# Kernel optimization log

Hardware: AMD Instinct MI355X
Metric: run time of the kernel (lower is better)

## Reference

```python
import jax, jax.numpy as jnp
import numpy as np

B, C, H, W = 8, 64, 64, 64
OUT_H, OUT_W = 32, 32


def setup_inputs() -> dict:
    key = jax.random.key(0)
    ks = jax.random.split(key, 9)
    s = 1.0 / np.sqrt(C).astype(np.float32)
    return {
        "x": jax.random.normal(ks[0], (B, C, H, W), jnp.float32),
        "wq": jax.random.normal(ks[1], (C, C), jnp.float32) * s,
        "bq": jax.random.normal(ks[2], (C,), jnp.float32) * 0.01,
        "wk": jax.random.normal(ks[3], (C, C), jnp.float32) * s,
        "bk": jax.random.normal(ks[4], (C,), jnp.float32) * 0.01,
        "wv": jax.random.normal(ks[5], (C, C), jnp.float32) * s,
        "bv": jax.random.normal(ks[6], (C,), jnp.float32) * 0.01,
        "wm": jax.random.normal(ks[7], (C, C), jnp.float32) * s,
        "bm": jax.random.normal(ks[8], (C,), jnp.float32) * 0.01,
    }


def reference(x, wq, bq, wk, bk, wv, bv, wm, bm):
    # pushforward: self-attention over spatial tokens, 1x1-conv mixing + ReLU,
    # then bilinear resize to out_shape (align_corners=False semantics).
    b, c, h, w = x.shape
    t = x.reshape(b, c, h * w).transpose(0, 2, 1)  # [B, HW, C] tokens
    q = jnp.einsum('bnc,dc->bnd', t, wq) + bq      # 1x1 conv == per-pixel linear
    k = jnp.einsum('bnc,dc->bnd', t, wk) + bk
    v = jnp.einsum('bnc,dc->bnd', t, wv) + bv
    scores = jnp.einsum('bnc,bmc->bnm', q, k) / jnp.sqrt(jnp.float32(c))  # [B, HW, HW]
    attn = jax.nn.softmax(scores, axis=-1)
    o = jnp.einsum('bnm,bmc->bnc', attn, v)        # [B, HW, C]
    mixed = jax.nn.relu(jnp.einsum('bnc,dc->bnd', o, wm) + bm)
    out = mixed.transpose(0, 2, 1).reshape(b, c, h, w)
    # F.interpolate(mode='bilinear', align_corners=False) == half-pixel bilinear, no antialias
    out = jax.image.resize(out, (b, c, OUT_H, OUT_W), method='bilinear', antialias=False)
    return out
```

## Files before the change

kernel.cpp:

```cpp
#include <hip/hip_runtime.h>
#include <stdint.h>

typedef unsigned short u16;
typedef unsigned int   u32;
typedef __attribute__((ext_vector_type(8)))  short short8;
typedef __attribute__((ext_vector_type(4)))  float f32x4;
typedef __attribute__((ext_vector_type(16))) float f32x16;

#define NTOK 4096
#define LOG2E 1.44269504088896340736f
#define QS    (0.125f * LOG2E)

__device__ __forceinline__ u16 f2bf(float f) {
    u32 u = __builtin_bit_cast(u32, f);
    u += 0x7fffu + ((u >> 16) & 1u);
    return (u16)(u >> 16);
}
__device__ __forceinline__ float bf2f(u16 v) {
    return __builtin_bit_cast(float, (u32)v << 16);
}
__device__ __forceinline__ u32 pk_hu(float a, float b) {
    u32 ua = __builtin_bit_cast(u32, a) + 0x8000u;
    u32 ub = __builtin_bit_cast(u32, b) + 0x8000u;
    return __builtin_amdgcn_perm(ub, ua, 0x07060302);
}
__device__ __forceinline__ f32x16 zero16() {
    f32x16 v;
#pragma unroll
    for (int i = 0; i < 16; ++i) v[i] = 0.f;
    return v;
}

#define MFMA16x32 __builtin_amdgcn_mfma_f32_16x16x32_bf16
#define MFMA32x16 __builtin_amdgcn_mfma_f32_32x32x16_bf16

__global__ __launch_bounds__(256) void qkv_mfma4(
    const float* __restrict__ x,
    const float* __restrict__ wq, const float* __restrict__ bq,
    const float* __restrict__ wk, const float* __restrict__ bk,
    const float* __restrict__ wv, const float* __restrict__ bv,
    u16* __restrict__ Q, u16* __restrict__ K, u16* __restrict__ Vp)
{
    __shared__ __align__(16) u16 Wl[3 * 64 * 72];
    __shared__ __align__(16) u16 Xl[64 * 64];
    const int tid  = threadIdx.x;
    const int b    = blockIdx.x & 7;
    const int slab = blockIdx.x >> 3;
    const int n0   = slab << 6;
    const int wave = tid >> 6;
    const int lane = tid & 63;
    const int quad = lane >> 4;
    const int l15  = lane & 15;

#pragma unroll
    for (int j = 0; j < 12; ++j) {
        const float* src = (j < 4) ? wq : (j < 8) ? wk : wv;
        const float sc = (j < 4) ? QS : 1.0f;
        const int idx = (j & 3) * 1024 + tid * 4;
        const float4 v = *(const float4*)(src + idx);
        uint2 pk;
        pk.x = (u32)f2bf(v.x * sc) | ((u32)f2bf(v.y * sc) << 16);
        pk.y = (u32)f2bf(v.z * sc) | ((u32)f2bf(v.w * sc) << 16);
        *(uint2*)&Wl[(j >> 2) * 4608 + (idx >> 6) * 72 + (idx & 63)] = pk;
    }

    float4 xs[4];
#pragma unroll
    for (int g = 0; g < 4; ++g) {
        const int ch = g * 16 + wave * 4 + quad;
        xs[g] = *(const float4*)(x + ((size_t)(b * 64 + ch)) * NTOK + n0 + l15 * 4);
    }
#pragma unroll
    for (int g = 0; g < 4; ++g) {
        const int ch = g * 16 + wave * 4 + quad;
        const float vv[4] = {xs[g].x, xs[g].y, xs[g].z, xs[g].w};
#pragma unroll
        for (int e = 0; e < 4; ++e) {
            const int tok = l15 * 4 + e;
            Xl[tok * 64 + (((ch >> 3) ^ (tok & 7)) & 7) * 8 + (ch & 7)] = f2bf(vv[e]);
        }
    }
    __syncthreads();

    const int row0 = wave * 16 + l15;
    short8 xf[2];
#pragma unroll
    for (int kk = 0; kk < 2; ++kk)
        xf[kk] = *(const short8*)&Xl[row0 * 64 + (((kk * 4 + quad) ^ (row0 & 7)) & 7) * 8];

    const size_t tokbase = (size_t)b * NTOK + n0 + wave * 16;

#pragma unroll
    for (int mat = 0; mat < 2; ++mat) {
        const float* bias = (mat == 0) ? bq : bk;
        const float bsc = (mat == 0) ? QS : 1.0f;
#pragma unroll
        for (int mt = 0; mt < 4; ++mt) {
            const u16* wr = &Wl[mat * 4608 + (mt * 16 + l15) * 72 + quad * 8];
            const short8 wf0 = *(const short8*)(wr);
            const short8 wf1 = *(const short8*)(wr + 32);
            f32x4 acc = {0.f, 0.f, 0.f, 0.f};
            acc = MFMA16x32(wf0, xf[0], acc, 0, 0, 0);
            acc = MFMA16x32(wf1, xf[1], acc, 0, 0, 0);
            const float4 b4 = *(const float4*)(bias + mt * 16 + quad * 4);
            uint2 pk;
            pk.x = (u32)f2bf(acc[0] + b4.x * bsc) | ((u32)f2bf(acc[1] + b4.y * bsc) << 16);
            pk.y = (u32)f2bf(acc[2] + b4.z * bsc) | ((u32)f2bf(acc[3] + b4.w * bsc) << 16);
            u16* dst = (mat == 0) ? Q : K;
            *(uint2*)(dst + (tokbase + l15) * 64 + mt * 16 + quad * 4) = pk;
        }
    }

    __syncthreads();
    u16* Vl = Xl;
    const int tok = wave * 16 + l15;
#pragma unroll
    for (int mt = 0; mt < 4; ++mt) {
        const u16* wr = &Wl[2 * 4608 + (mt * 16 + l15) * 72 + quad * 8];
        const short8 wf0 = *(const short8*)(wr);
        const short8 wf1 = *(const short8*)(wr + 32);
        f32x4 acc = {0.f, 0.f, 0.f, 0.f};
        acc = MFMA16x32(wf0, xf[0], acc, 0, 0, 0);
        acc = MFMA16x32(wf1, xf[1], acc, 0, 0, 0);
        const float4 b4 = *(const float4*)(bv + mt * 16 + quad * 4);
        const float o[4] = {acc[0] + b4.x, acc[1] + b4.y, acc[2] + b4.z, acc[3] + b4.w};
#pragma unroll
        for (int r = 0; r < 4; ++r) {
            const int d = mt * 16 + quad * 4 + r;
            Vl[d * 64 + (((tok >> 3) ^ ((d >> 1) & 7)) & 7) * 8 + (tok & 7)] = f2bf(o[r]);
        }
    }
    __syncthreads();

#pragma unroll
    for (int dd = 0; dd < 4; ++dd) {
        const int d2   = (tid >> 4) + dd * 16;
        const int tok0 = (tid & 15) * 4;
        const int slot = ((tok0 >> 3) ^ ((d2 >> 1) & 7)) & 7;
        const uint2 v2 = *(const uint2*)&Vl[d2 * 64 + slot * 8 + (tok0 & 7)];
        const int gt = slab * 2 + (tok0 >> 5);
        *(uint2*)(Vp + (((size_t)b * 128 + gt) * 64 + d2) * 32 + (tok0 & 31)) = v2;
    }
}

__global__ __launch_bounds__(512, 2) void attn7(
    const u16* __restrict__ Q, const u16* __restrict__ K,
    const u16* __restrict__ Vp,
    const float* __restrict__ wm, const float* __restrict__ bm,
    float* __restrict__ out)
{
    __shared__ __align__(16) char smem[54272];
    const int tid  = threadIdx.x;
    const int wave = tid >> 6;
    const int lane = tid & 63;
    const int c31  = lane & 31;
    const int hw   = lane >> 5;
    const int quad = lane >> 4;
    const int l15  = lane & 15;
    const int h    = wave >> 2;
    const int s    = wave & 3;
    const int b    = blockIdx.x & 7;
    const int oh   = blockIdx.x >> 3;
    const int n0   = oh * 128;

    short8 qf[2][4];
#pragma unroll
    for (int nt = 0; nt < 2; ++nt)
#pragma unroll
        for (int ks = 0; ks < 4; ++ks)
            qf[nt][ks] = *(const short8*)(Q + ((size_t)(b * NTOK + n0 + h * 64 + nt * 32 + c31)) * 64
                                            + ks * 16 + hw * 8);

    const u16* Kb  = K + ((size_t)b * NTOK + s * 1024) * 64;
    const u16* Vbp = Vp + ((size_t)b * 128 + s * 32) * 2048;

    f32x16 O[2][2];
#pragma unroll
    for (int mt = 0; mt < 2; ++mt)
#pragma unroll
        for (int nt = 0; nt < 2; ++nt) O[mt][nt] = zero16();
    float lpa[2] = {0.f, 0.f};

    auto load_kv = [&](short8 (&kf)[4], short8 (&vf)[4], int t) {
        const int tc = (t < 32) ? t : 31;
        const u16* kt = Kb + (size_t)tc * 2048;
#pragma unroll
        for (int ks = 0; ks < 4; ++ks)
            kf[ks] = *(const short8*)(kt + c31 * 64 + ks * 16 + hw * 8);
        const u16* vt = Vbp + (size_t)tc * 2048;
#pragma unroll
        for (int mk = 0; mk < 4; ++mk)
            vf[mk] = *(const short8*)(vt + ((mk >> 1) * 32 + c31) * 32 + (mk & 1) * 16 + hw * 8);
    };

    auto tile_tail = [&](const f32x16 (&sv)[2], const short8 (&vf)[4]) {
#pragma unroll
        for (int nt = 0; nt < 2; ++nt) {
            float p[16];
#pragma unroll
            for (int r = 0; r < 16; ++r) p[r] = __builtin_amdgcn_exp2f(sv[nt][r]);
            lpa[nt] += (((p[0] + p[1]) + (p[2] + p[3])) + ((p[4] + p[5]) + (p[6] + p[7])))
                     + (((p[8] + p[9]) + (p[10] + p[11])) + ((p[12] + p[13]) + (p[14] + p[15])));
            u32 g[8];
#pragma unroll
            for (int gi = 0; gi < 8; ++gi) g[gi] = pk_hu(p[2 * gi], p[2 * gi + 1]);
            const u32 rA = __shfl_xor(hw ? g[0] : g[2], 32);
            const u32 rB = __shfl_xor(hw ? g[1] : g[3], 32);
            const u32 rC = __shfl_xor(hw ? g[4] : g[6], 32);
            const u32 rD = __shfl_xor(hw ? g[5] : g[7], 32);
            uint4 B0, B1;
            B0.x = hw ? rA : g[0];  B0.y = hw ? rB : g[1];
            B0.z = hw ? g[2] : rA;  B0.w = hw ? g[3] : rB;
            B1.x = hw ? rC : g[4];  B1.y = hw ? rD : g[5];
            B1.z = hw ? g[6] : rC;  B1.w = hw ? g[7] : rD;
            const short8 pb0 = __builtin_bit_cast(short8, B0);
            const short8 pb1 = __builtin_bit_cast(short8, B1);
            O[0][nt] = MFMA32x16(vf[0], pb0, O[0][nt], 0, 0, 0);
            O[0][nt] = MFMA32x16(vf[1], pb1, O[0][nt], 0, 0, 0);
            O[1][nt] = MFMA32x16(vf[2], pb0, O[1][nt], 0, 0, 0);
            O[1][nt] = MFMA32x16(vf[3], pb1, O[1][nt], 0, 0, 0);
        }
    };

    short8 kfA[4], vfA[4], kfB[4], vfB[4];
    load_kv(kfA, vfA, 0);

#pragma unroll 1
    for (int tt = 0; tt < 16; ++tt) {
        const int t0 = tt * 2;
        f32x16 sv0[2];
#pragma unroll
        for (int nt = 0; nt < 2; ++nt) {
            f32x16 a = zero16();
            a = MFMA32x16(kfA[0], qf[nt][0], a, 0, 0, 0);
            a = MFMA32x16(kfA[1], qf[nt][1], a, 0, 0, 0);
            a = MFMA32x16(kfA[2], qf[nt][2], a, 0, 0, 0);
            a = MFMA32x16(kfA[3], qf[nt][3], a, 0, 0, 0);
            sv0[nt] = a;
        }
        load_kv(kfB, vfB, t0 + 1);
        tile_tail(sv0, vfA);

        f32x16 sv1[2];
#pragma unroll
        for (int nt = 0; nt < 2; ++nt) {
            f32x16 a = zero16();
            a = MFMA32x16(kfB[0], qf[nt][0], a, 0, 0, 0);
            a = MFMA32x16(kfB[1], qf[nt][1], a, 0, 0, 0);
            a = MFMA32x16(kfB[2], qf[nt][2], a, 0, 0, 0);
            a = MFMA32x16(kfB[3], qf[nt][3], a, 0, 0, 0);
            sv1[nt] = a;
        }
        load_kv(kfA, vfA, t0 + 2);
        tile_tail(sv1, vfB);
    }

#pragma unroll
    for (int nt = 0; nt < 2; ++nt) lpa[nt] += __shfl_xor(lpa[nt], 32);

    float* lpbuf = (float*)(smem + 52224);
    if (hw == 0) {
#pragma unroll
        for (int nt = 0; nt < 2; ++nt)
            lpbuf[(h * 4 + s) * 64 + nt * 32 + c31] = lpa[nt];
    }
    if (s != 0) {
        u16* sec = (u16*)smem + (h * 3 + s - 1) * 4352;
#pragma unroll
        for (int mt = 0; mt < 2; ++mt)
#pragma unroll
            for (int nt = 0; nt < 2; ++nt)
#pragma unroll
                for (int r = 0; r < 16; ++r) {
                    const int ch = mt * 32 + (r & 3) + 8 * (r >> 2) + 4 * hw;
                    sec[(nt * 32 + c31) * 68 + ch] = f2bf(O[mt][nt][r]);
                }
    }
    __syncthreads();

    float rinv[2];
    if (s == 0) {
#pragma unroll
        for (int nt = 0; nt < 2; ++nt) {
            float sum = 0.f;
#pragma unroll
            for (int sx = 0; sx < 4; ++sx)
                sum += lpbuf[(h * 4 + sx) * 64 + nt * 32 + c31];
            rinv[nt] = 1.0f / sum;
        }
#pragma unroll
        for (int sx = 1; sx < 4; ++sx) {
            const u16* sec = (const u16*)smem + (h * 3 + sx - 1) * 4352;
#pragma unroll
            for (int mt = 0; mt < 2; ++mt)
#pragma unroll
                for (int nt = 0; nt < 2; ++nt)
#pragma unroll
                    for (int r = 0; r < 16; ++r) {
                        const int ch = mt * 32 + (r & 3) + 8 * (r >> 2) + 4 * hw;
                        O[mt][nt][r] += bf2f(sec[(nt * 32 + c31) * 68 + ch]);
                    }
        }
    }
    short8 wB[4][2];
    float bb[4];
#pragma unroll
    for (int nt = 0; nt < 4; ++nt) {
        const int d = nt * 16 + l15;
        const float* wr = wm + (size_t)d * 64 + quad * 8;
        const float4 a0 = *(const float4*)(wr);
        const float4 a1 = *(const float4*)(wr + 4);
        const float4 c0 = *(const float4*)(wr + 32);
        const float4 c1 = *(const float4*)(wr + 36);
        ((u32*)&wB[nt][0])[0] = pk_hu(a0.y, a0.x) ^ 0u, ((u32*)&wB[nt][0])[0] = (u32)f2bf(a0.x) | ((u32)f2bf(a0.y) << 16);
        ((u32*)&wB[nt][0])[1] = (u32)f2bf(a0.z) | ((u32)f2bf(a0.w) << 16);
        ((u32*)&wB[nt][0])[2] = (u32)f2bf(a1.x) | ((u32)f2bf(a1.y) << 16);
        ((u32*)&wB[nt][0])[3] = (u32)f2bf(a1.z) | ((u32)f2bf(a1.w) << 16);
        ((u32*)&wB[nt][1])[0] = (u32)f2bf(c0.x) | ((u32)f2bf(c0.y) << 16);
        ((u32*)&wB[nt][1])[1] = (u32)f2bf(c0.z) | ((u32)f2bf(c0.w) << 16);
        ((u32*)&wB[nt][1])[2] = (u32)f2bf(c1.x) | ((u32)f2bf(c1.y) << 16);
        ((u32*)&wB[nt][1])[3] = (u32)f2bf(c1.z) | ((u32)f2bf(c1.w) << 16);
        bb[nt] = bm[d];
    }
    __syncthreads();

    if (s == 0) {
        u16* M0 = (u16*)smem + h * 4096;
#pragma unroll
        for (int mt = 0; mt < 2; ++mt)
#pragma unroll
            for (int nt = 0; nt < 2; ++nt)
#pragma unroll
                for (int r = 0; r < 16; ++r) {
                    const int lr = nt * 32 + c31;
                    const int ch = mt * 32 + (r & 3) + 8 * (r >> 2) + 4 * hw;
                    const float v = O[mt][nt][r] * rinv[nt];
                    M0[lr * 64 + (((ch >> 3) ^ (lr & 7)) & 7) * 8 + (ch & 7)] = f2bf(v);
                }
    }
    __syncthreads();

    const u16* M0r = (const u16*)smem + (wave >> 2) * 4096;
    const int lr = (wave & 3) * 16 + l15;
    const short8 af0 = *(const short8*)&M0r[lr * 64 + ((quad ^ (lr & 7)) & 7) * 8];
    const short8 af1 = *(const short8*)&M0r[lr * 64 + (((4 + quad) ^ (lr & 7)) & 7) * 8];
    float* Mf = (float*)(smem + 16384);
#pragma unroll
    for (int nt = 0; nt < 4; ++nt) {
        f32x4 acc = {0.f, 0.f, 0.f, 0.f};
        acc = MFMA16x32(af0, wB[nt][0], acc, 0, 0, 0);
        acc = MFMA16x32(af1, wB[nt][1], acc, 0, 0, 0);
#pragma unroll
        for (int r = 0; r < 4; ++r) {
            float v = acc[r] + bb[nt];
            v = v > 0.f ? v : 0.f;
            Mf[(wave * 16 + quad * 4 + r) * 68 + nt * 16 + l15] = v;
        }
    }
    __syncthreads();

    const int ow = tid & 31;
    const int cb = (tid >> 5) & 15;
#pragma unroll
    for (int i = 0; i < 4; ++i) {
        const int c = cb + i * 16;
        const float v = 0.25f * (Mf[(2 * ow) * 68 + c] + Mf[(2 * ow + 1) * 68 + c]
                               + Mf[(64 + 2 * ow) * 68 + c] + Mf[(65 + 2 * ow) * 68 + c]);
        out[((size_t)(b * 64 + c) * 32 + oh) * 32 + ow] = v;
    }
}

extern "C" void kernel_launch(void* const* d_in, const int* in_sizes, int n_in,
                              void* d_out, int out_size, void* d_ws, size_t ws_size,
                              hipStream_t stream) {
    (void)in_sizes; (void)n_in; (void)out_size; (void)ws_size;
    const float* x  = (const float*)d_in[0];
    const float* wq = (const float*)d_in[1];
    const float* bq = (const float*)d_in[2];
    const float* wk = (const float*)d_in[3];
    const float* bk = (const float*)d_in[4];
    const float* wv = (const float*)d_in[5];
    const float* bv = (const float*)d_in[6];
    const float* wm = (const float*)d_in[7];
    const float* bm = (const float*)d_in[8];

    u16* Q  = (u16*)d_ws;
    u16* K  = Q + (size_t)8 * NTOK * 64;
    u16* Vp = K + (size_t)8 * NTOK * 64;

    qkv_mfma4<<<512, 256, 0, stream>>>(x, wq, bq, wk, bk, wv, bv, Q, K, Vp);
    attn7<<<256, 512, 0, stream>>>(Q, K, Vp, wm, bm, (float*)d_out);
}
```

Baseline: 137.2 us.

## Split KV sequence across eight waves per query group with 1024-thread blocks

Doubles the block to 1024 threads so each query group's key/value sequence is split eight ways instead of four, halving per-wave loop length and doubling waves in flight. The split-K reduction, softmax normalization and output-mixing stages are reworked for the larger block, and LDS stores/loads become packed 64-bit. Per-block LDS rises to about 123KB, so occupancy is limited to one block per CU, and the serial reduction over seven partial sums by wave 0 grows.

```diff
diff --git a/kernel.cpp b/kernel.cpp
--- a/kernel.cpp
+++ b/kernel.cpp
@@ -143,13 +143,13 @@
     }
 }
 
-__global__ __launch_bounds__(512, 2) void attn7(
+__global__ __launch_bounds__(1024, 4) void attn8(
     const u16* __restrict__ Q, const u16* __restrict__ K,
     const u16* __restrict__ Vp,
     const float* __restrict__ wm, const float* __restrict__ bm,
     float* __restrict__ out)
 {
-    __shared__ __align__(16) char smem[54272];
+    __shared__ __align__(16) char smem[125952];
     const int tid  = threadIdx.x;
     const int wave = tid >> 6;
     const int lane = tid & 63;
@@ -157,8 +157,8 @@
     const int hw   = lane >> 5;
     const int quad = lane >> 4;
     const int l15  = lane & 15;
-    const int h    = wave >> 2;
-    const int s    = wave & 3;
+    const int h    = wave >> 3;
+    const int s    = wave & 7;
     const int b    = blockIdx.x & 7;
     const int oh   = blockIdx.x >> 3;
     const int n0   = oh * 128;
@@ -171,8 +171,8 @@
             qf[nt][ks] = *(const short8*)(Q + ((size_t)(b * NTOK + n0 + h * 64 + nt * 32 + c31)) * 64
                                             + ks * 16 + hw * 8);
 
-    const u16* Kb  = K + ((size_t)b * NTOK + s * 1024) * 64;
-    const u16* Vbp = Vp + ((size_t)b * 128 + s * 32) * 2048;
+    const u16* Kb  = K + ((size_t)b * NTOK + s * 512) * 64;
+    const u16* Vbp = Vp + ((size_t)b * 128 + s * 16) * 2048;
 
     f32x16 O[2][2];
 #pragma unroll
@@ -182,7 +182,7 @@
     float lpa[2] = {0.f, 0.f};
 
     auto load_kv = [&](short8 (&kf)[4], short8 (&vf)[4], int t) {
-        const int tc = (t < 32) ? t : 31;
+        const int tc = (t < 16) ? t : 15;
         const u16* kt = Kb + (size_t)tc * 2048;
 #pragma unroll
         for (int ks = 0; ks < 4; ++ks)
@@ -226,7 +226,7 @@
     load_kv(kfA, vfA, 0);
 
 #pragma unroll 1
-    for (int tt = 0; tt < 16; ++tt) {
+    for (int tt = 0; tt < 8; ++tt) {
         const int t0 = tt * 2;
         f32x16 sv0[2];
 #pragma unroll
@@ -258,22 +258,26 @@
 #pragma unroll
     for (int nt = 0; nt < 2; ++nt) lpa[nt] += __shfl_xor(lpa[nt], 32);
 
-    float* lpbuf = (float*)(smem + 52224);
+    float* lpbuf = (float*)(smem + 121856);
     if (hw == 0) {
 #pragma unroll
         for (int nt = 0; nt < 2; ++nt)
-            lpbuf[(h * 4 + s) * 64 + nt * 32 + c31] = lpa[nt];
+            lpbuf[(h * 8 + s) * 64 + nt * 32 + c31] = lpa[nt];
     }
     if (s != 0) {
-        u16* sec = (u16*)smem + (h * 3 + s - 1) * 4352;
+        u16* sec = (u16*)smem + (h * 7 + s - 1) * 4352;
 #pragma unroll
         for (int mt = 0; mt < 2; ++mt)
 #pragma unroll
             for (int nt = 0; nt < 2; ++nt)
 #pragma unroll
-                for (int r = 0; r < 16; ++r) {
-                    const int ch = mt * 32 + (r & 3) + 8 * (r >> 2) + 4 * hw;
-                    sec[(nt * 32 + c31) * 68 + ch] = f2bf(O[mt][nt][r]);
+                for (int rg = 0; rg < 4; ++rg) {
+                    const int row = nt * 32 + c31;
+                    const int ch0 = mt * 32 + rg * 8 + hw * 4;
+                    uint2 pk;
+                    pk.x = (u32)f2bf(O[mt][nt][rg * 4 + 0]) | ((u32)f2bf(O[mt][nt][rg * 4 + 1]) << 16);
+                    pk.y = (u32)f2bf(O[mt][nt][rg * 4 + 2]) | ((u32)f2bf(O[mt][nt][rg * 4 + 3]) << 16);
+                    *(uint2*)&sec[row * 68 + ch0] = pk;
                 }
     }
     __syncthreads();
@@ -284,86 +288,97 @@
         for (int nt = 0; nt < 2; ++nt) {
             float sum = 0.f;
 #pragma unroll
-            for (int sx = 0; sx < 4; ++sx)
-                sum += lpbuf[(h * 4 + sx) * 64 + nt * 32 + c31];
+            for (int sx = 0; sx < 8; ++sx)
+                sum += lpbuf[(h * 8 + sx) * 64 + nt * 32 + c31];
             rinv[nt] = 1.0f / sum;
         }
-#pragma unroll
-        for (int sx = 1; sx < 4; ++sx) {
-            const u16* sec = (const u16*)smem + (h * 3 + sx - 1) * 4352;
+#pragma unroll 1
+        for (int sx = 1; sx < 8; ++sx) {
+            const u16* sec = (const u16*)smem + (h * 7 + sx - 1) * 4352;
 #pragma unroll
             for (int mt = 0; mt < 2; ++mt)
 #pragma unroll
                 for (int nt = 0; nt < 2; ++nt)
 #pragma unroll
-                    for (int r = 0; r < 16; ++r) {
-                        const int ch = mt * 32 + (r & 3) + 8 * (r >> 2) + 4 * hw;
-                        O[mt][nt][r] += bf2f(sec[(nt * 32 + c31) * 68 + ch]);
+                    for (int rg = 0; rg < 4; ++rg) {
+                        const uint2 v = *(const uint2*)&sec[(nt * 32 + c31) * 68 + mt * 32 + rg * 8 + hw * 4];
+                        O[mt][nt][rg * 4 + 0] += bf2f((u16)v.x);
+                        O[mt][nt][rg * 4 + 1] += bf2f((u16)(v.x >> 16));
+                        O[mt][nt][rg * 4 + 2] += bf2f((u16)v.y);
+                        O[mt][nt][rg * 4 + 3] += bf2f((u16)(v.y >> 16));
                     }
         }
     }
-    short8 wB[4][2];
-    float bb[4];
-#pragma unroll
-    for (int nt = 0; nt < 4; ++nt) {
-        const int d = nt * 16 + l15;
+    const int rg8 = wave & 7;
+    const int ng  = wave >> 3;
+    short8 wB[2][2];
+    float bb[2];
+#pragma unroll
+    for (int j = 0; j < 2; ++j) {
+        const int d = (ng * 2 + j) * 16 + l15;
         const float* wr = wm + (size_t)d * 64 + quad * 8;
         const float4 a0 = *(const float4*)(wr);
         const float4 a1 = *(const float4*)(wr + 4);
         const float4 c0 = *(const float4*)(wr + 32);
         const float4 c1 = *(const float4*)(wr + 36);
-        ((u32*)&wB[nt][0])[0] = pk_hu(a0.y, a0.x) ^ 0u, ((u32*)&wB[nt][0])[0] = (u32)f2bf(a0.x) | ((u32)f2bf(a0.y) << 16);
-        ((u32*)&wB[nt][0])[1] = (u32)f2bf(a0.z) | ((u32)f2bf(a0.w) << 16);
-        ((u32*)&wB[nt][0])[2] = (u32)f2bf(a1.x) | ((u32)f2bf(a1.y) << 16);
-        ((u32*)&wB[nt][0])[3] = (u32)f2bf(a1.z) | ((u32)f2bf(a1.w) << 16);
-        ((u32*)&wB[nt][1])[0] = (u32)f2bf(c0.x) | ((u32)f2bf(c0.y) << 16);
-        ((u32*)&wB[nt][1])[1] = (u32)f2bf(c0.z) | ((u32)f2bf(c0.w) << 16);
-        ((u32*)&wB[nt][1])[2] = (u32)f2bf(c1.x) | ((u32)f2bf(c1.y) << 16);
-        ((u32*)&wB[nt][1])[3] = (u32)f2bf(c1.z) | ((u32)f2bf(c1.w) << 16);
-        bb[nt] = bm[d];
+        ((u32*)&wB[j][0])[0] = (u32)f2bf(a0.x) | ((u32)f2bf(a0.y) << 16);
+        ((u32*)&wB[j][0])[1] = (u32)f2bf(a0.z) | ((u32)f2bf(a0.w) << 16);
+        ((u32*)&wB[j][0])[2] = (u32)f2bf(a1.x) | ((u32)f2bf(a1.y) << 16);
+        ((u32*)&wB[j][0])[3] = (u32)f2bf(a1.z) | ((u32)f2bf(a1.w) << 16);
+        ((u32*)&wB[j][1])[0] = (u32)f2bf(c0.x) | ((u32)f2bf(c0.y) << 16);
+        ((u32*)&wB[j][1])[1] = (u32)f2bf(c0.z) | ((u32)f2bf(c0.w) << 16);
+        ((u32*)&wB[j][1])[2] = (u32)f2bf(c1.x) | ((u32)f2bf(c1.y) << 16);
+        ((u32*)&wB[j][1])[3] = (u32)f2bf(c1.z) | ((u32)f2bf(c1.w) << 16);
+        bb[j] = bm[d];
     }
     __syncthreads();
 
     if (s == 0) {
-        u16* M0 = (u16*)smem + h * 4096;
+        u16* M0 = (u16*)smem;
 #pragma unroll
         for (int mt = 0; mt < 2; ++mt)
 #pragma unroll
             for (int nt = 0; nt < 2; ++nt)
 #pragma unroll
-                for (int r = 0; r < 16; ++r) {
-                    const int lr = nt * 32 + c31;
-                    const int ch = mt * 32 + (r & 3) + 8 * (r >> 2) + 4 * hw;
-                    const float v = O[mt][nt][r] * rinv[nt];
-                    M0[lr * 64 + (((ch >> 3) ^ (lr & 7)) & 7) * 8 + (ch & 7)] = f2bf(v);
+                for (int rg = 0; rg < 4; ++rg) {
+                    const int lr  = h * 64 + nt * 32 + c31;
+                    const int ch0 = mt * 32 + rg * 8 + hw * 4;
+                    const int slot = ((ch0 >> 3) ^ (lr & 7)) & 7;
+                    uint2 pk;
+                    pk.x = (u32)f2bf(O[mt][nt][rg * 4 + 0] * rinv[nt])
+                         | ((u32)f2bf(O[mt][nt][rg * 4 + 1] * rinv[nt]) << 16);
+                    pk.y = (u32)f2bf(O[mt][nt][rg * 4 + 2] * rinv[nt])
+                         | ((u32)f2bf(O[mt][nt][rg * 4 + 3] * rinv[nt]) << 16);
+                    *(uint2*)&M0[lr * 64 + slot * 8 + hw * 4] = pk;
                 }
     }
     __syncthreads();
 
-    const u16* M0r = (const u16*)smem + (wave >> 2) * 4096;
-    const int lr = (wave & 3) * 16 + l15;
-    const short8 af0 = *(const short8*)&M0r[lr * 64 + ((quad ^ (lr & 7)) & 7) * 8];
-    const short8 af1 = *(const short8*)&M0r[lr * 64 + (((4 + quad) ^ (lr & 7)) & 7) * 8];
+    const u16* M0 = (const u16*)smem;
+    const int gr = rg8 * 16 + l15;
+    const short8 af0 = *(const short8*)&M0[gr * 64 + ((quad ^ (gr & 7)) & 7) * 8];
+    const short8 af1 = *(const short8*)&M0[gr * 64 + (((4 + quad) ^ (gr & 7)) & 7) * 8];
     float* Mf = (float*)(smem + 16384);
 #pragma unroll
-    for (int nt = 0; nt < 4; ++nt) {
+    for (int j = 0; j < 2; ++j) {
+        const int nt = ng * 2 + j;
         f32x4 acc = {0.f, 0.f, 0.f, 0.f};
-        acc = MFMA16x32(af0, wB[nt][0], acc, 0, 0, 0);
-        acc = MFMA16x32(af1, wB[nt][1], acc, 0, 0, 0);
+        acc = MFMA16x32(af0, wB[j][0], acc, 0, 0, 0);
+        acc = MFMA16x32(af1, wB[j][1], acc, 0, 0, 0);
 #pragma unroll
         for (int r = 0; r < 4; ++r) {
-            float v = acc[r] + bb[nt];
+            float v = acc[r] + bb[j];
             v = v > 0.f ? v : 0.f;
-            Mf[(wave * 16 + quad * 4 + r) * 68 + nt * 16 + l15] = v;
+            Mf[(rg8 * 16 + quad * 4 + r) * 68 + nt * 16 + l15] = v;
         }
     }
     __syncthreads();
 
     const int ow = tid & 31;
-    const int cb = (tid >> 5) & 15;
-#pragma unroll
-    for (int i = 0; i < 4; ++i) {
-        const int c = cb + i * 16;
+    const int cb = tid >> 5;
+#pragma unroll
+    for (int i = 0; i < 2; ++i) {
+        const int c = cb + i * 32;
         const float v = 0.25f * (Mf[(2 * ow) * 68 + c] + Mf[(2 * ow + 1) * 68 + c]
                                + Mf[(64 + 2 * ow) * 68 + c] + Mf[(65 + 2 * ow) * 68 + c]);
         out[((size_t)(b * 64 + c) * 32 + oh) * 32 + ow] = v;
@@ -389,5 +404,5 @@
     u16* Vp = K + (size_t)8 * NTOK * 64;
 
     qkv_mfma4<<<512, 256, 0, stream>>>(x, wq, bq, wk, bk, wv, bv, Q, K, Vp);
-    attn7<<<256, 512, 0, stream>>>(Q, K, Vp, wm, bm, (float*)d_out);
-}
+    attn8<<<256, 1024, 0, stream>>>(Q, K, Vp, wm, bm, (float*)d_out);
+}
```

Result: slower. 304.8 us (+122.2%).
